# Performance work log

Hardware: AMD Instinct MI355X
Metric: run time of the kernel (lower is better)

## Reference

```python
import jax, jax.numpy as jnp
import numpy as np


def setup_inputs() -> dict:
    key = jax.random.key(0)
    k1, k2 = jax.random.split(key)
    B, H, W, D, K = 32, 64, 64, 64, 512
    inputs = jax.random.normal(k1, (B, H, W, D), dtype=jnp.float32)
    # codebook: (D, K) as in the keras layer (embedding_dim x num_embeddings)
    embeddings = jax.random.uniform(k2, (D, K), dtype=jnp.float32,
                                    minval=-1.0, maxval=1.0) * (3.0 / D) ** 0.5
    return {"inputs": inputs, "embeddings": embeddings}


def reference(inputs, embeddings):
    # inputs: [B, H, W, D]; embeddings: [D, K]
    D = inputs.shape[-1]
    flat = inputs.reshape(-1, D)                                   # [N, D]
    distances = (jnp.sum(flat * flat, axis=1, keepdims=True)
                 - 2.0 * (flat @ embeddings)
                 + jnp.sum(embeddings * embeddings, axis=0, keepdims=True))
    encoding_indices = jnp.argmin(distances, axis=1)               # [N]
    encoding_indices = encoding_indices.reshape(inputs.shape[:-1])  # [B, H, W]
    quantized = jnp.take(embeddings.T, encoding_indices, axis=0)   # [B, H, W, D]
    # straight-through estimator
    return inputs + jax.lax.stop_gradient(quantized - inputs)
```

## Files before the change

### kernel.cpp

```cpp
#include <hip/hip_runtime.h>


#define KC 512
#define DD 64
#define TAU 5e-4f
#define HTAU (0.5f * TAU)

typedef __attribute__((ext_vector_type(8))) short short8;
typedef __attribute__((ext_vector_type(4))) float float4v;

__device__ inline unsigned short f2bf(float f) {
    unsigned u = __float_as_uint(f);
    return (unsigned short)((u + 0x7FFF + ((u >> 16) & 1)) >> 16);
}
__device__ inline float bf2f(unsigned short b) {
    return __uint_as_float((unsigned)b << 16);
}

__global__ __launch_bounds__(256) void vq_prep(const float* __restrict__ emb,
                                               float* __restrict__ et,
                                               float* __restrict__ bias,
                                               short* __restrict__ Bh,
                                               short* __restrict__ Bl) {
    __shared__ float tile[DD][17];
    const int ct = blockIdx.x;
    const int t  = threadIdx.x;

    {
        const int d = t >> 2, c0 = (t & 3) * 4;
        float4 v = *(const float4*)(emb + (size_t)d * KC + ct * 16 + c0);
        tile[d][c0 + 0] = v.x; tile[d][c0 + 1] = v.y;
        tile[d][c0 + 2] = v.z; tile[d][c0 + 3] = v.w;
    }
    __syncthreads();

    if (t < 16) {
        float s = 0.f;
        #pragma unroll
        for (int d = 0; d < DD; ++d) { float v = tile[d][t]; s += v * v; }
        bias[ct * 16 + t] = s;
    }

    {
        const int c = t >> 4, d0 = (t & 15) * 4;
        float4 v;
        v.x = tile[d0 + 0][c]; v.y = tile[d0 + 1][c];
        v.z = tile[d0 + 2][c]; v.w = tile[d0 + 3][c];
        *(float4*)(et + (size_t)(ct * 16 + c) * DD + d0) = v;
    }

    {
        const int term = t >> 7;
        const int kc   = (t >> 6) & 1;
        const int l    = t & 63;
        const int c    = l & 15, dq = l >> 4;
        short v8[8];
        #pragma unroll
        for (int j = 0; j < 8; ++j) {
            float f = tile[kc * 32 + dq * 8 + j][c];
            unsigned short h = f2bf(f);
            v8[j] = (short)(term == 0 ? h : f2bf(f - bf2f(h)));
        }
        short* dst = (term == 0 ? Bh : Bl) + ((size_t)(ct * 2 + kc) * 64 + l) * 8;
        *(short8*)dst = *(short8*)v8;
    }
}

__global__ __launch_bounds__(1024, 4) void vq_main(const float* __restrict__ x_in,
                                                   const short* __restrict__ Bh,
                                                   const short* __restrict__ Bl,
                                                   const float* __restrict__ bias,
                                                   const float* __restrict__ et,
                                                   float* __restrict__ out) {
    __shared__ __align__(16) short Bh_lds[32 * 2 * 64 * 8];
    __shared__ __align__(16) short Bl_lds[32 * 2 * 64 * 8];
    __shared__ float bias_s[KC];
    __shared__ int   k1s[16][32];
    __shared__ float gaps[16][32];

    const int t = threadIdx.x, w = t >> 6, l = t & 63;
    const int col = l & 15, quad = l >> 4;
    const int R0 = blockIdx.x * 512;
    const int wrow0 = w * 32;

    {
        const float4* srcH = (const float4*)Bh;
        const float4* srcL = (const float4*)Bl;
        float4* dstH = (float4*)Bh_lds;
        float4* dstL = (float4*)Bl_lds;
        #pragma unroll
        for (int j = 0; j < 4; ++j) {
            const int idx = t + j * 1024;
            dstH[idx] = srcH[idx];
            dstL[idx] = srcL[idx];
        }
        if (t < KC) bias_s[t] = bias[t];
    }

    short8 AH[2][2], AL[2][2];
    #pragma unroll
    for (int rt = 0; rt < 2; ++rt)
        #pragma unroll
        for (int kc = 0; kc < 2; ++kc) {
            const float* p = x_in + (size_t)(R0 + wrow0 + rt * 16 + col) * DD
                           + kc * 32 + quad * 8;
            float4 xa = *(const float4*)p;
            float4 xb = *(const float4*)(p + 4);
            float f[8] = {xa.x, xa.y, xa.z, xa.w, xb.x, xb.y, xb.z, xb.w};
            short8 hi8, lo8;
            #pragma unroll
            for (int j = 0; j < 8; ++j) {
                unsigned short h = f2bf(f[j]);
                hi8[j] = (short)h;
                lo8[j] = (short)f2bf(f[j] - bf2f(h));
            }
            AH[rt][kc] = hi8;
            AL[rt][kc] = lo8;
        }
    __syncthreads();

    float m1[2][4], m2[2][4];
    int   kb[2][4];
    #pragma unroll
    for (int rt = 0; rt < 2; ++rt)
        #pragma unroll
        for (int r = 0; r < 4; ++r) {
            m1[rt][r] = -3.4e38f; m2[rt][r] = -3.4e38f; kb[rt][r] = 0;
        }

    #pragma unroll 2
    for (int ct = 0; ct < 32; ++ct) {
        short8 bh0 = *(const short8*)&Bh_lds[((ct * 2 + 0) * 64 + l) * 8];
        short8 bh1 = *(const short8*)&Bh_lds[((ct * 2 + 1) * 64 + l) * 8];
        short8 bl0 = *(const short8*)&Bl_lds[((ct * 2 + 0) * 64 + l) * 8];
        short8 bl1 = *(const short8*)&Bl_lds[((ct * 2 + 1) * 64 + l) * 8];
        const float ci = -0.5f * bias_s[ct * 16 + col];
        const int kk = ct * 16 + col;
        #pragma unroll
        for (int rt = 0; rt < 2; ++rt) {
            float4v c = {ci, ci, ci, ci};
            c = __builtin_amdgcn_mfma_f32_16x16x32_bf16(AH[rt][0], bh0, c, 0, 0, 0);
            c = __builtin_amdgcn_mfma_f32_16x16x32_bf16(AH[rt][1], bh1, c, 0, 0, 0);
            c = __builtin_amdgcn_mfma_f32_16x16x32_bf16(AL[rt][0], bh0, c, 0, 0, 0);
            c = __builtin_amdgcn_mfma_f32_16x16x32_bf16(AL[rt][1], bh1, c, 0, 0, 0);
            c = __builtin_amdgcn_mfma_f32_16x16x32_bf16(AH[rt][0], bl0, c, 0, 0, 0);
            c = __builtin_amdgcn_mfma_f32_16x16x32_bf16(AH[rt][1], bl1, c, 0, 0, 0);
            #pragma unroll
            for (int r = 0; r < 4; ++r) {
                float cr = c[r];
                bool gt = cr > m1[rt][r];
                m2[rt][r] = fmaxf(fminf(cr, m1[rt][r]), m2[rt][r]);
                kb[rt][r] = gt ? kk : kb[rt][r];
                m1[rt][r] = fmaxf(m1[rt][r], cr);
            }
        }
    }

    #pragma unroll
    for (int rt = 0; rt < 2; ++rt)
        #pragma unroll
        for (int r = 0; r < 4; ++r) {
            float b1 = m1[rt][r], b2 = m2[rt][r];
            int   bk = kb[rt][r];
            #pragma unroll
            for (int m = 1; m <= 8; m <<= 1) {
                float o1 = __shfl_xor(b1, m, 64);
                float o2 = __shfl_xor(b2, m, 64);
                int   ok = __shfl_xor(bk, m, 64);
                float n2 = fmaxf(fmaxf(b2, o2), fminf(b1, o1));
                bool take = (o1 > b1) || (o1 == b1 && ok < bk);
                b1 = take ? o1 : b1;
                bk = take ? ok : bk;
                b2 = n2;
            }
            if (col == 0) {
                const int rowl = rt * 16 + quad * 4 + r;
                k1s[w][rowl]  = bk;
                gaps[w][rowl] = b1 - b2;
            }
        }
    __syncthreads();

    {
        unsigned long long mask = __ballot((l < 32) && (gaps[w][l] <= HTAU));
        while (mask) {
            const int rr = __builtin_ctzll(mask);
            mask &= mask - 1;
            const size_t grow = (size_t)(R0 + wrow0 + rr) * DD;
            const int kbase = l * 8;
            float acc[8];
            #pragma unroll
            for (int j = 0; j < 8; ++j) acc[j] = 0.f;
            for (int d0 = 0; d0 < DD; d0 += 4) {
                float4 xv = *(const float4*)(x_in + grow + d0);
                #pragma unroll
                for (int j = 0; j < 8; ++j) {
                    float4 ev = *(const float4*)(et + (size_t)(kbase + j) * DD + d0);
                    acc[j] += xv.x * ev.x;
                    acc[j] += xv.y * ev.y;
                    acc[j] += xv.z * ev.z;
                    acc[j] += xv.w * ev.w;
                }
            }
            float4 b0 = *(const float4*)(bias + kbase);
            float4 b1v = *(const float4*)(bias + kbase + 4);
            float bb[8] = {b0.x, b0.y, b0.z, b0.w, b1v.x, b1v.y, b1v.z, b1v.w};
            float bv = 3.4e38f; int bk = 0;
            #pragma unroll
            for (int j = 0; j < 8; ++j) {
                float s = bb[j] - 2.f * acc[j];
                if (s < bv) { bv = s; bk = kbase + j; }
            }
            #pragma unroll
            for (int m = 1; m <= 32; m <<= 1) {
                float ov = __shfl_xor(bv, m, 64);
                int   ok = __shfl_xor(bk, m, 64);
                if (ov < bv || (ov == bv && ok < bk)) { bv = ov; bk = ok; }
            }
            if (l == 0) k1s[w][rr] = bk;
        }
    }

    {
        const int c4 = col * 4;
        #pragma unroll
        for (int i = 0; i < 8; ++i) {
            const int rowl = i * 4 + quad;
            const int bk = k1s[w][rowl];
            float4 v = *(const float4*)(et + (size_t)bk * DD + c4);
            *(float4*)(out + (size_t)(R0 + wrow0 + rowl) * DD + c4) = v;
        }
    }
}

extern "C" void kernel_launch(void* const* d_in, const int* in_sizes, int n_in,
                              void* d_out, int out_size, void* d_ws, size_t ws_size,
                              hipStream_t stream) {
    const float* x_in = (const float*)d_in[0];
    const float* emb  = (const float*)d_in[1];
    float* out = (float*)d_out;

    float* et   = (float*)d_ws;
    float* bias = et + KC * DD;
    short* Bh   = (short*)(bias + KC);
    short* Bl   = Bh + 32 * 2 * 64 * 8;

    const int N = out_size / DD;

    vq_prep<<<32, 256, 0, stream>>>(emb, et, bias, Bh, Bl);
    vq_main<<<N / 512, 1024, 0, stream>>>(x_in, Bh, Bl, bias, et, out);
}
```

Baseline: 126.4 us.

## Use single-pass fp16 MFMA with per-row rigorous error bound for fallback

Replaces the three-term bf16 split product (hi*hi, lo*hi, hi*lo) with a single fp16 MFMA pass. This cuts matrix instructions per tile from six to two and halves the codebook LDS footprint. A new small kernel computes per-dimension max codebook magnitude and fp16 rounding error, and each row gets an error bound that widens the top-2 gap check. Rows whose gap falls within the bound are recomputed exactly in fp32. The block size also shrinks to 512 threads over 256 rows. The risk is more rows falling back to the scalar fp32 path, plus one extra tiny serial kernel launch.

```diff
diff --git a/kernel.cpp b/kernel.cpp
--- a/kernel.cpp
+++ b/kernel.cpp
@@ -3,25 +3,35 @@
 
 #define KC 512
 #define DD 64
-#define TAU 5e-4f
-#define HTAU (0.5f * TAU)
+#define MARGIN 2.5e-4f
 
 typedef __attribute__((ext_vector_type(8))) short short8;
+typedef _Float16 half8 __attribute__((ext_vector_type(8)));
 typedef __attribute__((ext_vector_type(4))) float float4v;
 
-__device__ inline unsigned short f2bf(float f) {
-    unsigned u = __float_as_uint(f);
-    return (unsigned short)((u + 0x7FFF + ((u >> 16) & 1)) >> 16);
-}
-__device__ inline float bf2f(unsigned short b) {
-    return __uint_as_float((unsigned)b << 16);
+__global__ __launch_bounds__(64) void vq_eps(const float* __restrict__ emb,
+                                             float* __restrict__ emax,
+                                             float* __restrict__ lemax) {
+    const int d = threadIdx.x;
+    float em = 0.f, lm = 0.f;
+    for (int k = 0; k < KC; k += 4) {
+        float4 v = *(const float4*)(emb + (size_t)d * KC + k);
+        float f[4] = {v.x, v.y, v.z, v.w};
+        #pragma unroll
+        for (int j = 0; j < 4; ++j) {
+            _Float16 h = (_Float16)f[j];
+            em = fmaxf(em, fabsf(f[j]));
+            lm = fmaxf(lm, fabsf(f[j] - (float)h));
+        }
+    }
+    emax[d]  = em;
+    lemax[d] = lm;
 }
 
 __global__ __launch_bounds__(256) void vq_prep(const float* __restrict__ emb,
                                                float* __restrict__ et,
                                                float* __restrict__ bias,
-                                               short* __restrict__ Bh,
-                                               short* __restrict__ Bl) {
+                                               short* __restrict__ Bf) {
     __shared__ float tile[DD][17];
     const int ct = blockIdx.x;
     const int t  = threadIdx.x;
@@ -49,55 +59,64 @@
         *(float4*)(et + (size_t)(ct * 16 + c) * DD + d0) = v;
     }
 
-    {
-        const int term = t >> 7;
-        const int kc   = (t >> 6) & 1;
-        const int l    = t & 63;
-        const int c    = l & 15, dq = l >> 4;
+    if (t < 128) {
+        const int kc = t >> 6, l = t & 63;
+        const int c  = l & 15, dq = l >> 4;
         short v8[8];
         #pragma unroll
         for (int j = 0; j < 8; ++j) {
             float f = tile[kc * 32 + dq * 8 + j][c];
-            unsigned short h = f2bf(f);
-            v8[j] = (short)(term == 0 ? h : f2bf(f - bf2f(h)));
-        }
-        short* dst = (term == 0 ? Bh : Bl) + ((size_t)(ct * 2 + kc) * 64 + l) * 8;
-        *(short8*)dst = *(short8*)v8;
-    }
-}
-
-__global__ __launch_bounds__(1024, 4) void vq_main(const float* __restrict__ x_in,
-                                                   const short* __restrict__ Bh,
-                                                   const short* __restrict__ Bl,
-                                                   const float* __restrict__ bias,
-                                                   const float* __restrict__ et,
-                                                   float* __restrict__ out) {
-    __shared__ __align__(16) short Bh_lds[32 * 2 * 64 * 8];
-    __shared__ __align__(16) short Bl_lds[32 * 2 * 64 * 8];
+            _Float16 h = (_Float16)f;
+            v8[j] = __builtin_bit_cast(short, h);
+        }
+        *(short8*)(Bf + ((size_t)(ct * 2 + kc) * 64 + l) * 8) = *(short8*)v8;
+    }
+}
+
+__global__ __launch_bounds__(512, 4) void vq_main(const float* __restrict__ x_in,
+                                                  const short* __restrict__ Bf,
+                                                  const float* __restrict__ bias,
+                                                  const float* __restrict__ emax,
+                                                  const float* __restrict__ lemax,
+                                                  const float* __restrict__ et,
+                                                  float* __restrict__ out) {
+    __shared__ __align__(16) short Bf_lds[32 * 2 * 64 * 8];
     __shared__ float bias_s[KC];
-    __shared__ int   k1s[16][32];
-    __shared__ float gaps[16][32];
+    __shared__ float eps_s[8][32];
+    __shared__ int   k1s[8][32];
+    __shared__ float gaps[8][32];
 
     const int t = threadIdx.x, w = t >> 6, l = t & 63;
     const int col = l & 15, quad = l >> 4;
-    const int R0 = blockIdx.x * 512;
+    const int R0 = blockIdx.x * 256;
     const int wrow0 = w * 32;
 
     {
-        const float4* srcH = (const float4*)Bh;
-        const float4* srcL = (const float4*)Bl;
-        float4* dstH = (float4*)Bh_lds;
-        float4* dstL = (float4*)Bl_lds;
-        #pragma unroll
-        for (int j = 0; j < 4; ++j) {
-            const int idx = t + j * 1024;
-            dstH[idx] = srcH[idx];
-            dstL[idx] = srcL[idx];
-        }
-        if (t < KC) bias_s[t] = bias[t];
-    }
-
-    short8 AH[2][2], AL[2][2];
+        const float4* src = (const float4*)Bf;
+        float4* dst = (float4*)Bf_lds;
+        #pragma unroll
+        for (int j = 0; j < 8; ++j) {
+            const int idx = t + j * 512;
+            dst[idx] = src[idx];
+        }
+        bias_s[t] = bias[t];
+    }
+
+    float em[2][8], lm[2][8];
+    #pragma unroll
+    for (int kc = 0; kc < 2; ++kc) {
+        float4 a = *(const float4*)(emax + kc * 32 + quad * 8);
+        float4 b = *(const float4*)(emax + kc * 32 + quad * 8 + 4);
+        em[kc][0] = a.x; em[kc][1] = a.y; em[kc][2] = a.z; em[kc][3] = a.w;
+        em[kc][4] = b.x; em[kc][5] = b.y; em[kc][6] = b.z; em[kc][7] = b.w;
+        float4 c = *(const float4*)(lemax + kc * 32 + quad * 8);
+        float4 d = *(const float4*)(lemax + kc * 32 + quad * 8 + 4);
+        lm[kc][0] = c.x; lm[kc][1] = c.y; lm[kc][2] = c.z; lm[kc][3] = c.w;
+        lm[kc][4] = d.x; lm[kc][5] = d.y; lm[kc][6] = d.z; lm[kc][7] = d.w;
+    }
+
+    half8 AF[2][2];
+    float errp[2] = {0.f, 0.f};
     #pragma unroll
     for (int rt = 0; rt < 2; ++rt)
         #pragma unroll
@@ -107,16 +126,24 @@
             float4 xa = *(const float4*)p;
             float4 xb = *(const float4*)(p + 4);
             float f[8] = {xa.x, xa.y, xa.z, xa.w, xb.x, xb.y, xb.z, xb.w};
-            short8 hi8, lo8;
             #pragma unroll
             for (int j = 0; j < 8; ++j) {
-                unsigned short h = f2bf(f[j]);
-                hi8[j] = (short)h;
-                lo8[j] = (short)f2bf(f[j] - bf2f(h));
-            }
-            AH[rt][kc] = hi8;
-            AL[rt][kc] = lo8;
-        }
+                _Float16 h = (_Float16)f[j];
+                AF[rt][kc][j] = h;
+                float fh = (float)h;
+                errp[rt] = fmaf(fabsf(f[j] - fh), em[kc][j], errp[rt]);
+                errp[rt] = fmaf(fabsf(fh),        lm[kc][j], errp[rt]);
+            }
+        }
+    #pragma unroll
+    for (int rt = 0; rt < 2; ++rt) {
+        errp[rt] += __shfl_xor(errp[rt], 16, 64);
+        errp[rt] += __shfl_xor(errp[rt], 32, 64);
+    }
+    if (quad == 0) {
+        eps_s[w][col]      = errp[0];
+        eps_s[w][16 + col] = errp[1];
+    }
     __syncthreads();
 
     float m1[2][4], m2[2][4];
@@ -130,21 +157,15 @@
 
     #pragma unroll 2
     for (int ct = 0; ct < 32; ++ct) {
-        short8 bh0 = *(const short8*)&Bh_lds[((ct * 2 + 0) * 64 + l) * 8];
-        short8 bh1 = *(const short8*)&Bh_lds[((ct * 2 + 1) * 64 + l) * 8];
-        short8 bl0 = *(const short8*)&Bl_lds[((ct * 2 + 0) * 64 + l) * 8];
-        short8 bl1 = *(const short8*)&Bl_lds[((ct * 2 + 1) * 64 + l) * 8];
+        half8 bf0 = *(const half8*)&Bf_lds[((ct * 2 + 0) * 64 + l) * 8];
+        half8 bf1 = *(const half8*)&Bf_lds[((ct * 2 + 1) * 64 + l) * 8];
         const float ci = -0.5f * bias_s[ct * 16 + col];
         const int kk = ct * 16 + col;
         #pragma unroll
         for (int rt = 0; rt < 2; ++rt) {
             float4v c = {ci, ci, ci, ci};
-            c = __builtin_amdgcn_mfma_f32_16x16x32_bf16(AH[rt][0], bh0, c, 0, 0, 0);
-            c = __builtin_amdgcn_mfma_f32_16x16x32_bf16(AH[rt][1], bh1, c, 0, 0, 0);
-            c = __builtin_amdgcn_mfma_f32_16x16x32_bf16(AL[rt][0], bh0, c, 0, 0, 0);
-            c = __builtin_amdgcn_mfma_f32_16x16x32_bf16(AL[rt][1], bh1, c, 0, 0, 0);
-            c = __builtin_amdgcn_mfma_f32_16x16x32_bf16(AH[rt][0], bl0, c, 0, 0, 0);
-            c = __builtin_amdgcn_mfma_f32_16x16x32_bf16(AH[rt][1], bl1, c, 0, 0, 0);
+            c = __builtin_amdgcn_mfma_f32_16x16x32_f16(AF[rt][0], bf0, c, 0, 0, 0);
+            c = __builtin_amdgcn_mfma_f32_16x16x32_f16(AF[rt][1], bf1, c, 0, 0, 0);
             #pragma unroll
             for (int r = 0; r < 4; ++r) {
                 float cr = c[r];
@@ -176,13 +197,13 @@
             if (col == 0) {
                 const int rowl = rt * 16 + quad * 4 + r;
                 k1s[w][rowl]  = bk;
-                gaps[w][rowl] = b1 - b2;
-            }
-        }
-    __syncthreads();
-
-    {
-        unsigned long long mask = __ballot((l < 32) && (gaps[w][l] <= HTAU));
+                gaps[w][rowl] = (b1 - b2) - 2.f * eps_s[w][rowl];
+            }
+        }
+
+    {
+        unsigned long long mask = __ballot((l < 32) && (gaps[w][l & 31] <= MARGIN));
+        mask &= 0xFFFFFFFFull;
         while (mask) {
             const int rr = __builtin_ctzll(mask);
             mask &= mask - 1;
@@ -240,13 +261,15 @@
     const float* emb  = (const float*)d_in[1];
     float* out = (float*)d_out;
 
-    float* et   = (float*)d_ws;
-    float* bias = et + KC * DD;
-    short* Bh   = (short*)(bias + KC);
-    short* Bl   = Bh + 32 * 2 * 64 * 8;
+    float* et    = (float*)d_ws;
+    float* bias  = et + KC * DD;
+    short* Bf    = (short*)(bias + KC);
+    float* emax  = (float*)(Bf + 32 * 2 * 64 * 8);
+    float* lemax = emax + DD;
 
     const int N = out_size / DD;
 
-    vq_prep<<<32, 256, 0, stream>>>(emb, et, bias, Bh, Bl);
-    vq_main<<<N / 512, 1024, 0, stream>>>(x_in, Bh, Bl, bias, et, out);
-}
+    vq_eps<<<1, 64, 0, stream>>>(emb, emax, lemax);
+    vq_prep<<<32, 256, 0, stream>>>(emb, et, bias, Bf);
+    vq_main<<<N / 256, 512, 0, stream>>>(x_in, Bf, bias, emax, lemax, et, out);
+}
```

Result: slower. 284.5 us (+125.1%).
